# Kernel tuning notes

Measured on AMD Instinct MI355X. Metric: run time of the kernel, lower is better.

## Reference

```python
import jax, jax.numpy as jnp
import numpy as np

NEG_CLAMP = -100.0  # torch F.binary_cross_entropy clamps log terms at -100


def _ccl_labels(fg):
    """4-connectivity connected-component labeling of a [H,W] bool mask.
    Labels are assigned in raster-scan first-encounter order, matching
    scipy.ndimage.label with the default structure. Background = 0.
    Implemented as min-index label propagation to a fixed point: each
    component ends up tagged with the min flat index of its pixels (its
    first raster-scan pixel), then roots are ranked by cumsum to get 1..num.
    """
    H, W = fg.shape
    INF = H * W  # sentinel larger than any flat index
    idx = jnp.arange(INF, dtype=jnp.int32).reshape(H, W)
    init = jnp.where(fg, idx, INF)

    def step(x):
        up = jnp.concatenate([x[1:], jnp.full((1, W), INF, x.dtype)], axis=0)
        down = jnp.concatenate([jnp.full((1, W), INF, x.dtype), x[:-1]], axis=0)
        left = jnp.concatenate([x[:, 1:], jnp.full((H, 1), INF, x.dtype)], axis=1)
        right = jnp.concatenate([jnp.full((H, 1), INF, x.dtype), x[:, :-1]], axis=1)
        m = jnp.minimum(jnp.minimum(up, down), jnp.minimum(left, right))
        return jnp.where(fg, jnp.minimum(x, m), INF)

    def cond(carry):
        return carry[1]

    def body(carry):
        x, _ = carry
        nx = step(x)
        return nx, jnp.any(nx != x)

    x, _ = jax.lax.while_loop(cond, body, (init, jnp.array(True)))

    flat = x.reshape(-1)
    fgf = fg.reshape(-1)
    # a pixel is the root of its component iff its propagated tag == its own index
    is_root = fgf & (flat == jnp.arange(INF, dtype=jnp.int32))
    rank = jnp.cumsum(is_root.astype(jnp.int32))  # rank[r] = scipy label of root r
    labels = jnp.where(fgf, rank[jnp.clip(flat, 0, INF - 1)], 0)
    return labels.reshape(H, W)


def _target_map(fg):
    """Replicates: labels == labels.flatten()[1:].argmax() + 1 (faithful to source,
    including its quirky use of argmax position as the selected label value)."""
    labels = _ccl_labels(fg)
    lf = labels.reshape(-1)
    v = jnp.argmax(lf[1:]) + 1  # first occurrence of max, like numpy argmax
    return (labels == v).astype(jnp.float32)


def setup_inputs() -> dict:
    key = jax.random.key(0)
    pred = jax.random.uniform(key, (32, 1, 512, 512), dtype=jnp.float32)
    return {"pred": pred}


def reference(pred):
    fg = pred[:, 0] >= 0.5  # [N,H,W] bool
    target = jax.vmap(_target_map)(fg)[:, None]  # [N,1,H,W] float
    logp = jnp.maximum(jnp.log(pred), NEG_CLAMP)
    log1mp = jnp.maximum(jnp.log1p(-pred), NEG_CLAMP)
    return -jnp.mean(target * logp + (1.0 - target) * log1mp)
```

## Files before the change

### kernel.cpp

```cpp
#include <hip/hip_runtime.h>
#include <math.h>

#define IMG_W 512
#define IMG_H 512
#define HW (IMG_W * IMG_H)
#define LOGHW 18
#define NIMG 32
#define NTOT (NIMG * HW)
#define TILE 64
#define TPI 64
#define NTILE (NIMG * TPI)
#define CPI 64
#define NSCHUNK (NIMG * CPI)
#define EDGE_N (NTILE * 64)
#define NPAIR (NIMG * 112)

__device__ __forceinline__ void uf_unite(int* L, int a, int b) {
    while (true) {
        int p = ((volatile int*)L)[a];
        while (p != a) { a = p; p = ((volatile int*)L)[a]; }
        p = ((volatile int*)L)[b];
        while (p != b) { b = p; p = ((volatile int*)L)[b]; }
        if (a == b) return;
        if (a < b) { int t = a; a = b; b = t; }
        int old = atomicMin(&L[a], b);
        if (old == a) return;
        a = old;
    }
}

__global__ __launch_bounds__(1024) void k_local(const float* __restrict__ pred,
                                                int* __restrict__ L,
                                                float* __restrict__ partials,
                                                int* __restrict__ edges,
                                                unsigned int* __restrict__ counter) {
    __shared__ int lab[TILE * TILE];
    __shared__ float sred[1024];
    int tile = blockIdx.x;
    int img = tile >> 6;
    int t = tile & (TPI - 1);
    int ty = t >> 3, tx = t & 7;
    int baseLocal = (ty * TILE) * IMG_W + tx * TILE;
    const float* pi = pred + ((size_t)img << LOGHW);
    int* Li = L + ((size_t)img << LOGHW);
    int tid = threadIdx.x;
    int lane = tid & 63, wave = tid >> 6;

    float pv[4];
#pragma unroll
    for (int j = 0; j < 4; j++) {
        int row = wave + j * 16;
        pv[j] = pi[baseLocal + row * IMG_W + lane];
    }
    float acc = 0.0f;
    unsigned long long maskle = (~0ULL) >> (63 - lane);
#pragma unroll
    for (int j = 0; j < 4; j++) {
        int row = wave + j * 16;
        float p = pv[j];
        acc += fmaxf(__logf(1.0f - p), -100.0f);
        bool fg = (p >= 0.5f);
        unsigned long long bal = __ballot(fg);
        unsigned long long starts = bal & ~(bal << 1);
        int lb = -1;
        if (fg) {
            unsigned long long pre = starts & maskle;
            lb = row * TILE + (63 - __builtin_clzll(pre));
        }
        lab[row * TILE + lane] = lb;
    }
    __syncthreads();
#pragma unroll
    for (int j = 0; j < 4; j++) {
        int row = wave + j * 16;
        if (row == 0) continue;
        int i = row * TILE + lane;
        bool c = (lab[i] >= 0) && (lab[i - TILE] >= 0);
        unsigned long long cb = __ballot(c);
        unsigned long long cs = cb & ~(cb << 1);
        if ((cs >> lane) & 1ULL) uf_unite(lab, i, i - TILE);
    }
    __syncthreads();
#pragma unroll
    for (int j = 0; j < 4; j++) {
        int row = wave + j * 16;
        int i = row * TILE + lane;
        bool fg = (lab[i] >= 0);
        unsigned long long bal = __ballot(fg);
        unsigned long long st = bal & ~(bal << 1);
        if ((st >> lane) & 1ULL) {
            int x = i, p = lab[x];
            while (p != x) {
                int g = lab[p];
                lab[x] = g;
                x = g;
                p = lab[x];
            }
            lab[i] = x;
        }
    }
    __syncthreads();
    {
        int i4 = tid * 4;
        int ly = i4 >> 6, lx = i4 & 63;
        int4 o;
        int* op = (int*)&o;
#pragma unroll
        for (int k = 0; k < 4; k++) {
            int s = lab[i4 + k];
            if (s < 0) op[k] = -1;
            else {
                int r = lab[s];
                op[k] = baseLocal + (r >> 6) * IMG_W + (r & 63);
            }
        }
        *(int4*)(Li + baseLocal + ly * IMG_W + lx) = o;
    }
    if (tid < 256) {
        int e = tid >> 6;
        int q = tid & 63;
        int px = (e == 0) ? q
               : (e == 1) ? (63 * TILE + q)
               : (e == 2) ? (q * TILE)
               :            (q * TILE + 63);
        int s = lab[px];
        int val = -1;
        if (s >= 0) {
            int r = lab[s];
            val = baseLocal + (r >> 6) * IMG_W + (r & 63);
        }
        edges[e * EDGE_N + tile * 64 + q] = val;
    }
    sred[tid] = acc;
    __syncthreads();
    for (int s = 512; s > 0; s >>= 1) {
        if (tid < s) sred[tid] += sred[tid + s];
        __syncthreads();
    }
    if (tid == 0) partials[blockIdx.x] = sred[0];
    if (blockIdx.x == 0 && tid == 0) *counter = 0u;
}

__global__ __launch_bounds__(256) void k_border(const int* __restrict__ edges,
                                                int* __restrict__ L) {
    int gid = blockIdx.x * blockDim.x + threadIdx.x;
    int pair = gid >> 6;
    int lane = gid & 63;
    int a, b, img;
    if (pair < NIMG * 56) {
        img = pair / 56;
        int w = pair - img * 56;
        int ty = w / 7, tx = w - ty * 7;
        int tl = img * TPI + ty * 8 + tx;
        a = edges[3 * EDGE_N + tl * 64 + lane];
        b = edges[2 * EDGE_N + (tl + 1) * 64 + lane];
    } else {
        int p2 = pair - NIMG * 56;
        img = p2 / 56;
        int w = p2 - img * 56;
        int ty = w >> 3, tx = w & 7;
        int tu = img * TPI + ty * 8 + tx;
        a = edges[1 * EDGE_N + tu * 64 + lane];
        b = edges[0 * EDGE_N + (tu + 8) * 64 + lane];
    }
    bool c = (a >= 0) && (b >= 0);
    unsigned long long cb = __ballot(c);
    unsigned long long cs = cb & ~(cb << 1);
    if ((cs >> lane) & 1ULL)
        uf_unite(L + ((size_t)img << LOGHW), a, b);
}

__global__ __launch_bounds__(256) void k_stats(const int* __restrict__ L,
                                               int* __restrict__ cntArr,
                                               int* __restrict__ maxArr,
                                               int* __restrict__ minArr) {
    __shared__ int s1[256], s2[256], s3[256];
    int chunk = blockIdx.x;
    int img = chunk >> 6;
    int baseL = (chunk & 63) * 4096;
    const int* Li = L + ((size_t)img << LOGHW);
    int t = threadIdx.x;
    int cnt = 0, mx = -1, mn = HW;
#pragma unroll
    for (int j = 0; j < 4; j++) {
        int off = baseL + (t + j * 256) * 4;
        int4 l4 = *(const int4*)(Li + off);
        const int* lp = (const int*)&l4;
#pragma unroll
        for (int k = 0; k < 4; k++) {
            int local = off + k;
            int p = lp[k];
            bool root = (p == local);
            cnt += root ? 1 : 0;
            if (root && local > mx) mx = local;
            if (p >= 0 && local >= 1 && local < mn) mn = local;
        }
    }
    s1[t] = cnt; s2[t] = mx; s3[t] = mn;
    __syncthreads();
    for (int s = 128; s > 0; s >>= 1) {
        if (t < s) {
            s1[t] += s1[t + s];
            s2[t] = max(s2[t], s2[t + s]);
            s3[t] = min(s3[t], s3[t + s]);
        }
        __syncthreads();
    }
    if (t == 0) { cntArr[chunk] = s1[0]; maxArr[chunk] = s2[0]; minArr[chunk] = s3[0]; }
}

__global__ __launch_bounds__(256) void k_tail(const int* __restrict__ cntArr,
                                              const int* __restrict__ maxArr,
                                              const int* __restrict__ minArr,
                                              const int* __restrict__ L,
                                              const float* __restrict__ pred,
                                              const float* __restrict__ partials,
                                              float* __restrict__ corr,
                                              unsigned int* __restrict__ counter,
                                              float* __restrict__ out) {
    __shared__ int sc[256], sm[256], sn[256];
    __shared__ int sel_chunk, sel_base, result;
    __shared__ float sf[256];
    __shared__ double sd[256];
    __shared__ unsigned int oldc;
    int img = blockIdx.x, t = threadIdx.x;
    const int* Li = L + ((size_t)img << LOGHW);
    int cnt = (t < CPI) ? cntArr[img * CPI + t] : 0;
    sc[t] = cnt;
    sm[t] = (t < CPI) ? maxArr[img * CPI + t] : -1;
    sn[t] = (t < CPI) ? minArr[img * CPI + t] : HW;
    if (t == 0) result = -2;
    __syncthreads();
    for (int off = 1; off < 256; off <<= 1) {
        int v2 = (t >= off) ? sc[t - off] : 0;
        __syncthreads();
        sc[t] += v2;
        __syncthreads();
    }
    int num = sc[255];
    int inc = sc[t], exc = inc - cnt;
    for (int s = 128; s > 0; s >>= 1) {
        if (t < s) { sm[t] = max(sm[t], sm[t + s]); sn[t] = min(sn[t], sn[t + s]); }
        __syncthreads();
    }
    int last_root = sm[0], minFg = sn[0];
    int v;
    if (last_root >= 1) v = last_root;
    else if (last_root == 0) v = (minFg < HW) ? minFg : 1;
    else v = 1;
    if (v >= 1 && v <= num) {
        if (exc < v && v <= inc) { sel_chunk = t; sel_base = exc; }
        __syncthreads();
        int c = sel_chunk, base = sel_base;
        int baseL = c * 4096;
        int f[16];
        int sum = 0;
#pragma unroll
        for (int j = 0; j < 4; j++) {
            int off = baseL + t * 16 + j * 4;
            int4 l4 = *(const int4*)(Li + off);
            const int* lp = (const int*)&l4;
#pragma unroll
            for (int k = 0; k < 4; k++) {
                f[j * 4 + k] = (lp[k] == off + k) ? 1 : 0;
                sum += f[j * 4 + k];
            }
        }
        __syncthreads();
        sc[t] = sum;
        __syncthreads();
        for (int off = 1; off < 256; off <<= 1) {
            int v2 = (t >= off) ? sc[t - off] : 0;
            __syncthreads();
            sc[t] += v2;
            __syncthreads();
        }
        int exc2 = sc[t] - sum;
        int need = v - base;
        if (exc2 < need && need <= sc[t]) {
            int run = exc2;
#pragma unroll
            for (int k = 0; k < 16; k++) {
                run += f[k];
                if (run == need) { result = baseL + t * 16 + k; break; }
            }
        }
        __syncthreads();
    } else {
        __syncthreads();
    }
    int rvv = result;
    float blocksum = 0.0f;
    if (rvv >= 0) {
        const float* pi = pred + ((size_t)img << LOGHW);
        float acc = 0.0f;
        for (int it = 0; it < HW / 1024; it++) {
            int off = it * 1024 + t * 4;
            float4 p4 = *(const float4*)(pi + off);
            int4 l4 = *(const int4*)(Li + off);
            const float* pp = (const float*)&p4;
            const int* lp = (const int*)&l4;
#pragma unroll
            for (int k = 0; k < 4; k++) {
                int p = lp[k];
                if (p < 0) continue;
                int x = p, q = Li[x];
                while (q != x) { x = q; q = Li[x]; }
                if (x == rvv) {
                    float pr = pp[k];
                    acc += fmaxf(__logf(pr), -100.0f)
                         - fmaxf(__logf(1.0f - pr), -100.0f);
                }
            }
        }
        sf[t] = acc;
        __syncthreads();
        for (int s = 128; s > 0; s >>= 1) {
            if (t < s) sf[t] += sf[t + s];
            __syncthreads();
        }
        blocksum = sf[0];
    }
    if (t == 0) {
        __hip_atomic_store(&corr[img], blocksum, __ATOMIC_RELAXED,
                           __HIP_MEMORY_SCOPE_AGENT);
        oldc = __hip_atomic_fetch_add(counter, 1u, __ATOMIC_ACQ_REL,
                                      __HIP_MEMORY_SCOPE_AGENT);
    }
    __syncthreads();
    if (oldc != NIMG - 1) return;
    double acc = 0.0;
#pragma unroll
    for (int j = 0; j < 8; j++) acc += (double)partials[t + j * 256];
    if (t < NIMG)
        acc += (double)__hip_atomic_load(&corr[t], __ATOMIC_ACQUIRE,
                                         __HIP_MEMORY_SCOPE_AGENT);
    sd[t] = acc;
    __syncthreads();
    for (int s = 128; s > 0; s >>= 1) {
        if (t < s) sd[t] += sd[t + s];
        __syncthreads();
    }
    if (t == 0) out[0] = (float)(-sd[0] / (double)NTOT);
}

extern "C" void kernel_launch(void* const* d_in, const int* in_sizes, int n_in,
                              void* d_out, int out_size, void* d_ws, size_t ws_size,
                              hipStream_t stream) {
    const float* pred = (const float*)d_in[0];
    float* out = (float*)d_out;

    char* ws = (char*)d_ws;
    int* L = (int*)ws;
    int* edges = (int*)(ws + (size_t)NTOT * 4);
    int* cntArr = edges + 4 * EDGE_N;
    int* maxArr = cntArr + NSCHUNK;
    int* minArr = maxArr + NSCHUNK;
    float* partials = (float*)(minArr + NSCHUNK);
    float* corr = partials + NTILE;
    unsigned int* counter = (unsigned int*)(corr + NIMG);

    k_local<<<dim3(NTILE), dim3(1024), 0, stream>>>(pred, L, partials, edges, counter);
    k_border<<<dim3(NPAIR * 64 / 256), dim3(256), 0, stream>>>(edges, L);
    k_stats<<<dim3(NSCHUNK), dim3(256), 0, stream>>>(L, cntArr, maxArr, minArr);
    k_tail<<<dim3(NIMG), dim3(256), 0, stream>>>(cntArr, maxArr, minArr, L, pred,
                                                 partials, corr, counter, out);
}
```

Baseline: 124.6 us.

## Keep per-row foreground bitmasks in shared memory and use wave-shuffle reduction

Stores each tile row's foreground ballot mask in shared memory and writes union-find labels only at run-start pixels. Later phases (vertical unions, path compression, output and edge writes) derive run starts from the masks instead of reading the per-pixel label array. The 1024-entry shared tree reduction is replaced by wave shuffles plus a 16-entry sum. This cuts shared-memory traffic and barriers in the local-labeling kernel, at the cost of extra bit arithmetic per pixel.

```diff
diff --git a/kernel.cpp b/kernel.cpp
--- a/kernel.cpp
+++ b/kernel.cpp
@@ -35,7 +35,8 @@
                                                 int* __restrict__ edges,
                                                 unsigned int* __restrict__ counter) {
     __shared__ int lab[TILE * TILE];
-    __shared__ float sred[1024];
+    __shared__ unsigned long long msk[TILE];
+    __shared__ float wsum[16];
     int tile = blockIdx.x;
     int img = tile >> 6;
     int t = tile & (TPI - 1);
@@ -61,34 +62,35 @@
         acc += fmaxf(__logf(1.0f - p), -100.0f);
         bool fg = (p >= 0.5f);
         unsigned long long bal = __ballot(fg);
+        if (lane == 0) msk[row] = bal;
         unsigned long long starts = bal & ~(bal << 1);
-        int lb = -1;
-        if (fg) {
-            unsigned long long pre = starts & maskle;
-            lb = row * TILE + (63 - __builtin_clzll(pre));
-        }
-        lab[row * TILE + lane] = lb;
+        if ((starts >> lane) & 1ULL)
+            lab[row * TILE + lane] = row * TILE + lane;
     }
     __syncthreads();
 #pragma unroll
     for (int j = 0; j < 4; j++) {
         int row = wave + j * 16;
         if (row == 0) continue;
-        int i = row * TILE + lane;
-        bool c = (lab[i] >= 0) && (lab[i - TILE] >= 0);
-        unsigned long long cb = __ballot(c);
-        unsigned long long cs = cb & ~(cb << 1);
-        if ((cs >> lane) & 1ULL) uf_unite(lab, i, i - TILE);
+        unsigned long long mc = msk[row], mu = msk[row - 1];
+        unsigned long long c = mc & mu;
+        unsigned long long cs = c & ~(c << 1);
+        if ((cs >> lane) & 1ULL) {
+            unsigned long long stc = mc & ~(mc << 1);
+            unsigned long long stu = mu & ~(mu << 1);
+            int a = row * TILE + (63 - __builtin_clzll(stc & maskle));
+            int b = (row - 1) * TILE + (63 - __builtin_clzll(stu & maskle));
+            uf_unite(lab, a, b);
+        }
     }
     __syncthreads();
 #pragma unroll
     for (int j = 0; j < 4; j++) {
         int row = wave + j * 16;
-        int i = row * TILE + lane;
-        bool fg = (lab[i] >= 0);
-        unsigned long long bal = __ballot(fg);
-        unsigned long long st = bal & ~(bal << 1);
+        unsigned long long m = msk[row];
+        unsigned long long st = m & ~(m << 1);
         if ((st >> lane) & 1ULL) {
+            int i = row * TILE + lane;
             int x = i, p = lab[x];
             while (p != x) {
                 int g = lab[p];
@@ -102,42 +104,72 @@
     __syncthreads();
     {
         int i4 = tid * 4;
-        int ly = i4 >> 6, lx = i4 & 63;
+        int row = i4 >> 6, lx = i4 & 63;
+        unsigned long long m = msk[row];
+        unsigned long long st = m & ~(m << 1);
         int4 o;
         int* op = (int*)&o;
 #pragma unroll
         for (int k = 0; k < 4; k++) {
-            int s = lab[i4 + k];
-            if (s < 0) op[k] = -1;
+            int l = lx + k;
+            if (!((m >> l) & 1ULL)) op[k] = -1;
             else {
+                unsigned long long pre = st & ((~0ULL) >> (63 - l));
+                int s = row * TILE + (63 - __builtin_clzll(pre));
                 int r = lab[s];
                 op[k] = baseLocal + (r >> 6) * IMG_W + (r & 63);
             }
         }
-        *(int4*)(Li + baseLocal + ly * IMG_W + lx) = o;
+        *(int4*)(Li + baseLocal + row * IMG_W + lx) = o;
     }
     if (tid < 256) {
         int e = tid >> 6;
         int q = tid & 63;
-        int px = (e == 0) ? q
-               : (e == 1) ? (63 * TILE + q)
-               : (e == 2) ? (q * TILE)
-               :            (q * TILE + 63);
-        int s = lab[px];
         int val = -1;
-        if (s >= 0) {
-            int r = lab[s];
-            val = baseLocal + (r >> 6) * IMG_W + (r & 63);
+        if (e == 0) {
+            unsigned long long m = msk[0];
+            if ((m >> q) & 1ULL) {
+                unsigned long long st = m & ~(m << 1);
+                int s = 63 - __builtin_clzll(st & ((~0ULL) >> (63 - q)));
+                int r = lab[s];
+                val = baseLocal + (r >> 6) * IMG_W + (r & 63);
+            }
+        } else if (e == 1) {
+            unsigned long long m = msk[63];
+            if ((m >> q) & 1ULL) {
+                unsigned long long st = m & ~(m << 1);
+                int s = 63 * TILE + (63 - __builtin_clzll(st & ((~0ULL) >> (63 - q))));
+                int r = lab[s];
+                val = baseLocal + (r >> 6) * IMG_W + (r & 63);
+            }
+        } else if (e == 2) {
+            unsigned long long m = msk[q];
+            if (m & 1ULL) {
+                int r = lab[q * TILE];
+                val = baseLocal + (r >> 6) * IMG_W + (r & 63);
+            }
+        } else {
+            unsigned long long m = msk[q];
+            if ((m >> 63) & 1ULL) {
+                unsigned long long st = m & ~(m << 1);
+                int s = q * TILE + (63 - __builtin_clzll(st));
+                int r = lab[s];
+                val = baseLocal + (r >> 6) * IMG_W + (r & 63);
+            }
         }
         edges[e * EDGE_N + tile * 64 + q] = val;
     }
-    sred[tid] = acc;
-    __syncthreads();
-    for (int s = 512; s > 0; s >>= 1) {
-        if (tid < s) sred[tid] += sred[tid + s];
-        __syncthreads();
-    }
-    if (tid == 0) partials[blockIdx.x] = sred[0];
+#pragma unroll
+    for (int off = 32; off > 0; off >>= 1)
+        acc += __shfl_down(acc, off, 64);
+    if (lane == 0) wsum[wave] = acc;
+    __syncthreads();
+    if (tid == 0) {
+        float s = 0.0f;
+#pragma unroll
+        for (int w = 0; w < 16; w++) s += wsum[w];
+        partials[blockIdx.x] = s;
+    }
     if (blockIdx.x == 0 && tid == 0) *counter = 0u;
 }
 
```

Result: no change. 124.3 us (-0.3%).

## Label 32x32 tiles per wavefront with run-length masks, no block barriers

Applied to the files above, without the earlier changes.

Local connected-component labeling now works on 32x32 tiles, one per wavefront, with four wavefronts per 256-thread block instead of one 64x64 tile per 1024-thread block. Each wave keeps per-row ballot bitmasks in shared memory and labels only run starts, uniting vertical run overlaps as it streams rows. This removes __syncthreads between phases and replaces the shared-memory tree reduction with wave shuffles. The trade-off is four times as many tile borders, so the global border-merge kernel does more union-find work across half-wave pairs, possibly with more atomic contention.

```diff
diff --git a/kernel.cpp b/kernel.cpp
--- a/kernel.cpp
+++ b/kernel.cpp
@@ -7,13 +7,16 @@
 #define LOGHW 18
 #define NIMG 32
 #define NTOT (NIMG * HW)
-#define TILE 64
-#define TPI 64
-#define NTILE (NIMG * TPI)
 #define CPI 64
 #define NSCHUNK (NIMG * CPI)
-#define EDGE_N (NTILE * 64)
-#define NPAIR (NIMG * 112)
+#define STILE 32
+#define TPI2 256
+#define NTILE2 (NIMG * TPI2)
+#define WPB 4
+#define NBLK2 (NTILE2 / WPB)
+#define EDGE2 (NTILE2 * 32)
+#define PPI 480
+#define NPAIR2 (NIMG * PPI)
 
 __device__ __forceinline__ void uf_unite(int* L, int a, int b) {
     while (true) {
@@ -29,143 +32,167 @@
     }
 }
 
-__global__ __launch_bounds__(1024) void k_local(const float* __restrict__ pred,
-                                                int* __restrict__ L,
-                                                float* __restrict__ partials,
-                                                int* __restrict__ edges,
-                                                unsigned int* __restrict__ counter) {
-    __shared__ int lab[TILE * TILE];
-    __shared__ float sred[1024];
-    int tile = blockIdx.x;
-    int img = tile >> 6;
-    int t = tile & (TPI - 1);
-    int ty = t >> 3, tx = t & 7;
-    int baseLocal = (ty * TILE) * IMG_W + tx * TILE;
+__global__ __launch_bounds__(256) void k_local(const float* __restrict__ pred,
+                                               int* __restrict__ L,
+                                               float* __restrict__ partials,
+                                               int* __restrict__ edges,
+                                               unsigned int* __restrict__ counter) {
+    __shared__ int lab[WPB * 1024];
+    __shared__ unsigned int mskS[WPB * 32];
+    __shared__ float wsum[WPB];
+    int tid = threadIdx.x;
+    int lane = tid & 63, wave = tid >> 6;
+    int tileG = blockIdx.x * WPB + wave;
+    int img = tileG >> 8;
+    int t = tileG & 255;
+    int ty = t >> 4, tx = t & 15;
+    int baseLocal = (ty * STILE) * IMG_W + tx * STILE;
     const float* pi = pred + ((size_t)img << LOGHW);
     int* Li = L + ((size_t)img << LOGHW);
-    int tid = threadIdx.x;
-    int lane = tid & 63, wave = tid >> 6;
-
-    float pv[4];
+    int* mylab = lab + wave * 1024;
+    unsigned int* mymsk = mskS + wave * 32;
+    int sub = lane >> 5;
+    int q = lane & 31;
+    unsigned int mle = 0xFFFFFFFFu >> (31 - q);
+
+    float acc = 0.0f;
+    unsigned int mprev = 0;
+    for (int i = 0; i < 16; i++) {
+        int row = 2 * i + sub;
+        float p = pi[baseLocal + row * IMG_W + q];
+        acc += fmaxf(__logf(1.0f - p), -100.0f);
+        unsigned long long bal = __ballot(p >= 0.5f);
+        unsigned int m0 = (unsigned int)bal;
+        unsigned int m1 = (unsigned int)(bal >> 32);
+        if (lane == 0)  mymsk[2 * i] = m0;
+        if (lane == 32) mymsk[2 * i + 1] = m1;
+        unsigned int m = sub ? m1 : m0;
+        unsigned int st = m & ~(m << 1);
+        if ((st >> q) & 1u) mylab[row * STILE + q] = row * STILE + q;
+        unsigned int mup = sub ? m0 : mprev;
+        unsigned int mdn = sub ? m1 : m0;
+        int rup = 2 * i - 1 + sub;
+        unsigned int cu = mup & mdn;
+        unsigned int cs = cu & ~(cu << 1);
+        if ((cs >> q) & 1u) {
+            unsigned int stup = mup & ~(mup << 1);
+            unsigned int stdn = mdn & ~(mdn << 1);
+            int a = rup * STILE + (31 - __builtin_clz(stup & mle));
+            int b = (rup + 1) * STILE + (31 - __builtin_clz(stdn & mle));
+            uf_unite(mylab, a, b);
+        }
+        mprev = m1;
+    }
+    for (int i = 0; i < 16; i++) {
+        int row = 2 * i + sub;
+        unsigned int m = mymsk[row];
+        unsigned int st = m & ~(m << 1);
+        if ((st >> q) & 1u) {
+            int idx = row * STILE + q;
+            int x = idx, p = mylab[x];
+            while (p != x) {
+                int g = mylab[p];
+                mylab[x] = g;
+                x = g;
+                p = mylab[x];
+            }
+            mylab[idx] = x;
+        }
+    }
 #pragma unroll
     for (int j = 0; j < 4; j++) {
-        int row = wave + j * 16;
-        pv[j] = pi[baseLocal + row * IMG_W + lane];
-    }
-    float acc = 0.0f;
-    unsigned long long maskle = (~0ULL) >> (63 - lane);
-#pragma unroll
-    for (int j = 0; j < 4; j++) {
-        int row = wave + j * 16;
-        float p = pv[j];
-        acc += fmaxf(__logf(1.0f - p), -100.0f);
-        bool fg = (p >= 0.5f);
-        unsigned long long bal = __ballot(fg);
-        unsigned long long starts = bal & ~(bal << 1);
-        int lb = -1;
-        if (fg) {
-            unsigned long long pre = starts & maskle;
-            lb = row * TILE + (63 - __builtin_clzll(pre));
-        }
-        lab[row * TILE + lane] = lb;
-    }
-    __syncthreads();
-#pragma unroll
-    for (int j = 0; j < 4; j++) {
-        int row = wave + j * 16;
-        if (row == 0) continue;
-        int i = row * TILE + lane;
-        bool c = (lab[i] >= 0) && (lab[i - TILE] >= 0);
-        unsigned long long cb = __ballot(c);
-        unsigned long long cs = cb & ~(cb << 1);
-        if ((cs >> lane) & 1ULL) uf_unite(lab, i, i - TILE);
-    }
-    __syncthreads();
-#pragma unroll
-    for (int j = 0; j < 4; j++) {
-        int row = wave + j * 16;
-        int i = row * TILE + lane;
-        bool fg = (lab[i] >= 0);
-        unsigned long long bal = __ballot(fg);
-        unsigned long long st = bal & ~(bal << 1);
-        if ((st >> lane) & 1ULL) {
-            int x = i, p = lab[x];
-            while (p != x) {
-                int g = lab[p];
-                lab[x] = g;
-                x = g;
-                p = lab[x];
-            }
-            lab[i] = x;
-        }
-    }
-    __syncthreads();
-    {
-        int i4 = tid * 4;
-        int ly = i4 >> 6, lx = i4 & 63;
+        int idx = (j * 64 + lane) * 4;
+        int row = idx >> 5, c0 = idx & 31;
+        unsigned int m = mymsk[row];
+        unsigned int st = m & ~(m << 1);
         int4 o;
         int* op = (int*)&o;
 #pragma unroll
         for (int k = 0; k < 4; k++) {
-            int s = lab[i4 + k];
-            if (s < 0) op[k] = -1;
+            int c = c0 + k;
+            if (!((m >> c) & 1u)) op[k] = -1;
             else {
-                int r = lab[s];
-                op[k] = baseLocal + (r >> 6) * IMG_W + (r & 63);
-            }
-        }
-        *(int4*)(Li + baseLocal + ly * IMG_W + lx) = o;
-    }
-    if (tid < 256) {
-        int e = tid >> 6;
-        int q = tid & 63;
-        int px = (e == 0) ? q
-               : (e == 1) ? (63 * TILE + q)
-               : (e == 2) ? (q * TILE)
-               :            (q * TILE + 63);
-        int s = lab[px];
+                unsigned int pre = st & (0xFFFFFFFFu >> (31 - c));
+                int s = row * STILE + (31 - __builtin_clz(pre));
+                int r = mylab[s];
+                op[k] = baseLocal + (r >> 5) * IMG_W + (r & 31);
+            }
+        }
+        *(int4*)(Li + baseLocal + row * IMG_W + c0) = o;
+    }
+#pragma unroll
+    for (int pass = 0; pass < 2; pass++) {
+        int e = pass * 2 + sub;
         int val = -1;
-        if (s >= 0) {
-            int r = lab[s];
-            val = baseLocal + (r >> 6) * IMG_W + (r & 63);
-        }
-        edges[e * EDGE_N + tile * 64 + q] = val;
-    }
-    sred[tid] = acc;
-    __syncthreads();
-    for (int s = 512; s > 0; s >>= 1) {
-        if (tid < s) sred[tid] += sred[tid + s];
-        __syncthreads();
-    }
-    if (tid == 0) partials[blockIdx.x] = sred[0];
+        if (e == 0) {
+            unsigned int m = mymsk[0];
+            if ((m >> q) & 1u) {
+                unsigned int st = m & ~(m << 1);
+                int s = 31 - __builtin_clz(st & mle);
+                int r = mylab[s];
+                val = baseLocal + (r >> 5) * IMG_W + (r & 31);
+            }
+        } else if (e == 1) {
+            unsigned int m = mymsk[31];
+            if ((m >> q) & 1u) {
+                unsigned int st = m & ~(m << 1);
+                int s = 31 * STILE + (31 - __builtin_clz(st & mle));
+                int r = mylab[s];
+                val = baseLocal + (r >> 5) * IMG_W + (r & 31);
+            }
+        } else if (e == 2) {
+            unsigned int m = mymsk[q];
+            if (m & 1u) {
+                int r = mylab[q * STILE];
+                val = baseLocal + (r >> 5) * IMG_W + (r & 31);
+            }
+        } else {
+            unsigned int m = mymsk[q];
+            if ((m >> 31) & 1u) {
+                unsigned int st = m & ~(m << 1);
+                int s = q * STILE + (31 - __builtin_clz(st));
+                int r = mylab[s];
+                val = baseLocal + (r >> 5) * IMG_W + (r & 31);
+            }
+        }
+        edges[e * EDGE2 + tileG * 32 + q] = val;
+    }
+#pragma unroll
+    for (int off = 32; off > 0; off >>= 1)
+        acc += __shfl_down(acc, off, 64);
+    if (lane == 0) wsum[wave] = acc;
+    __syncthreads();
+    if (tid == 0)
+        partials[blockIdx.x] = wsum[0] + wsum[1] + wsum[2] + wsum[3];
     if (blockIdx.x == 0 && tid == 0) *counter = 0u;
 }
 
 __global__ __launch_bounds__(256) void k_border(const int* __restrict__ edges,
                                                 int* __restrict__ L) {
     int gid = blockIdx.x * blockDim.x + threadIdx.x;
-    int pair = gid >> 6;
+    int w = gid >> 6;
     int lane = gid & 63;
-    int a, b, img;
-    if (pair < NIMG * 56) {
-        img = pair / 56;
-        int w = pair - img * 56;
-        int ty = w / 7, tx = w - ty * 7;
-        int tl = img * TPI + ty * 8 + tx;
-        a = edges[3 * EDGE_N + tl * 64 + lane];
-        b = edges[2 * EDGE_N + (tl + 1) * 64 + lane];
+    int pair = w * 2 + (lane >> 5);
+    int q = lane & 31;
+    int img = pair / PPI;
+    int r = pair - img * PPI;
+    int a, b;
+    if (r < 240) {
+        int ty = r / 15, tx = r - ty * 15;
+        int tl = img * TPI2 + ty * 16 + tx;
+        a = edges[3 * EDGE2 + tl * 32 + q];
+        b = edges[2 * EDGE2 + (tl + 1) * 32 + q];
     } else {
-        int p2 = pair - NIMG * 56;
-        img = p2 / 56;
-        int w = p2 - img * 56;
-        int ty = w >> 3, tx = w & 7;
-        int tu = img * TPI + ty * 8 + tx;
-        a = edges[1 * EDGE_N + tu * 64 + lane];
-        b = edges[0 * EDGE_N + (tu + 8) * 64 + lane];
+        int r2 = r - 240;
+        int ty = r2 >> 4, tx = r2 & 15;
+        int tu = img * TPI2 + ty * 16 + tx;
+        a = edges[1 * EDGE2 + tu * 32 + q];
+        b = edges[0 * EDGE2 + (tu + 16) * 32 + q];
     }
     bool c = (a >= 0) && (b >= 0);
     unsigned long long cb = __ballot(c);
-    unsigned long long cs = cb & ~(cb << 1);
+    unsigned long long shifted = (cb << 1) & ~(1ULL << 32);
+    unsigned long long cs = cb & ~shifted;
     if ((cs >> lane) & 1ULL)
         uf_unite(L + ((size_t)img << LOGHW), a, b);
 }
@@ -353,15 +380,15 @@
     char* ws = (char*)d_ws;
     int* L = (int*)ws;
     int* edges = (int*)(ws + (size_t)NTOT * 4);
-    int* cntArr = edges + 4 * EDGE_N;
+    int* cntArr = edges + 4 * EDGE2;
     int* maxArr = cntArr + NSCHUNK;
     int* minArr = maxArr + NSCHUNK;
     float* partials = (float*)(minArr + NSCHUNK);
-    float* corr = partials + NTILE;
+    float* corr = partials + NBLK2;
     unsigned int* counter = (unsigned int*)(corr + NIMG);
 
-    k_local<<<dim3(NTILE), dim3(1024), 0, stream>>>(pred, L, partials, edges, counter);
-    k_border<<<dim3(NPAIR * 64 / 256), dim3(256), 0, stream>>>(edges, L);
+    k_local<<<dim3(NBLK2), dim3(256), 0, stream>>>(pred, L, partials, edges, counter);
+    k_border<<<dim3(NPAIR2 * 32 / 256), dim3(256), 0, stream>>>(edges, L);
     k_stats<<<dim3(NSCHUNK), dim3(256), 0, stream>>>(L, cntArr, maxArr, minArr);
     k_tail<<<dim3(NIMG), dim3(256), 0, stream>>>(cntArr, maxArr, minArr, L, pred,
                                                  partials, corr, counter, out);
```

Result: faster. 121.3 us (-2.6%).
